# Kernel optimization log

Measured on AMD Instinct MI355X. Metric: run time of the kernel, lower is better.

The kernel has to match this reference:

```python
import jax, jax.numpy as jnp
import numpy as np

B, C, H, W = 2, 256, 360, 360
N1 = N2 = 1024


def setup_inputs() -> dict:
    key = jax.random.key(0)
    ks = jax.random.split(key, 12)
    s = 0.02
    feature = jax.random.normal(ks[0], (B, C, H, W), dtype=jnp.float32)
    # midx rows: [batch_idx, h, w]; frame 0 centers and frame 1 centers
    idx1 = jnp.stack([
        jnp.zeros((N1,), dtype=jnp.int32),
        jax.random.randint(ks[1], (N1,), 0, H, dtype=jnp.int32),
        jax.random.randint(ks[2], (N1,), 0, W, dtype=jnp.int32),
    ])
    idx2 = jnp.stack([
        jnp.ones((N2,), dtype=jnp.int32),
        jax.random.randint(ks[3], (N2,), 0, H, dtype=jnp.int32),
        jax.random.randint(ks[4], (N2,), 0, W, dtype=jnp.int32),
    ])
    w1 = jax.random.normal(ks[5], (256, 256), dtype=jnp.float32) * s
    b1 = jnp.zeros((256,), dtype=jnp.float32)
    w2 = jax.random.normal(ks[6], (256, 128), dtype=jnp.float32) * s
    b2 = jnp.zeros((128,), dtype=jnp.float32)
    w3 = jax.random.normal(ks[7], (128, 32), dtype=jnp.float32) * s
    b3 = jnp.zeros((32,), dtype=jnp.float32)
    w4 = jax.random.normal(ks[8], (32, 1), dtype=jnp.float32) * s
    b4 = jnp.zeros((1,), dtype=jnp.float32)
    return {"feature": feature, "idx1": idx1, "idx2": idx2,
            "w1": w1, "b1": b1, "w2": w2, "b2": b2,
            "w3": w3, "b3": b3, "w4": w4, "b4": b4}


def reference(feature, idx1, idx2, w1, b1, w2, b2, w3, b3, w4, b4):
    # feature: [B,C,H,W] -> [B,H,W,C] (torch .permute(0,2,3,1))
    feat = jnp.transpose(feature, (0, 2, 3, 1))

    def project(midx):
        # irregular gather of per-center features: [N, C]
        x = feat[midx[0], midx[1], midx[2]]
        h = jax.nn.relu(x @ w1 + b1)          # [N, 256]
        return jax.nn.relu(h @ w2 + b2)       # [N, 128]

    f1 = project(idx1)                        # [N1, D]
    f2 = project(idx2)                        # [N2, D]
    # laplacian_dists: broadcast outer difference [N1, N2, D]
    diff = f1[:, None, :] - f2[None, :, :]
    # out_layer = linear_last(D, 32, 1): Linear -> ReLU -> Linear
    h = jax.nn.relu(jnp.einsum('mnd,dk->mnk', diff, w3) + b3)
    out = jnp.einsum('mnk,ko->mno', h, w4) + b4
    return out[..., 0]                        # [N1, N2] similarity
```

## Files before the change

kernel.cpp:

```cpp
#include <hip/hip_runtime.h>

#define NPTS 1024
#define NC 256
#define NH 360
#define NW 360
#define NHW (NH * NW)
#define NCHW (NC * NHW)
#define PPB 4

__global__ __launch_bounds__(256) void mlp_kernel(
    const float* __restrict__ feature,
    const int* __restrict__ idx1,
    const int* __restrict__ idx2,
    const float* __restrict__ w1, const float* __restrict__ b1,
    const float* __restrict__ w2, const float* __restrict__ b2,
    const float* __restrict__ w3, const float* __restrict__ b3,
    float* __restrict__ pq)
{
    __shared__ float4 Xs[256];
    __shared__ float4 H1s[256];
    __shared__ float4 F2s[128];

    const int tid = threadIdx.x;
    const int base = blockIdx.x * PPB;

    {
        const int c = tid;
        const int col0 = base & (NPTS - 1);
        const int* idx = (base < NPTS) ? idx1 : idx2;
        const int4 bb4 = *(const int4*)(idx + col0);
        const int4 hh4 = *(const int4*)(idx + NPTS + col0);
        const int4 ww4 = *(const int4*)(idx + 2 * NPTS + col0);
        const size_t coff = (size_t)c * NHW;
        float4 v;
        v.x = __builtin_nontemporal_load(
                  feature + (size_t)bb4.x * NCHW + coff + (size_t)(hh4.x * NW + ww4.x));
        v.y = __builtin_nontemporal_load(
                  feature + (size_t)bb4.y * NCHW + coff + (size_t)(hh4.y * NW + ww4.y));
        v.z = __builtin_nontemporal_load(
                  feature + (size_t)bb4.z * NCHW + coff + (size_t)(hh4.z * NW + ww4.z));
        v.w = __builtin_nontemporal_load(
                  feature + (size_t)bb4.w * NCHW + coff + (size_t)(hh4.w * NW + ww4.w));
        Xs[c] = v;
    }
    __syncthreads();

    {
        const int j = tid;
        float4 acc = make_float4(0.f, 0.f, 0.f, 0.f);
        #pragma unroll 8
        for (int c = 0; c < 256; ++c) {
            const float wv = w1[c * 256 + j];
            const float4 a = Xs[c];
            acc.x = fmaf(a.x, wv, acc.x);
            acc.y = fmaf(a.y, wv, acc.y);
            acc.z = fmaf(a.z, wv, acc.z);
            acc.w = fmaf(a.w, wv, acc.w);
        }
        const float bj = b1[j];
        float4 h;
        h.x = fmaxf(acc.x + bj, 0.f);
        h.y = fmaxf(acc.y + bj, 0.f);
        h.z = fmaxf(acc.z + bj, 0.f);
        h.w = fmaxf(acc.w + bj, 0.f);
        H1s[j] = h;
    }
    __syncthreads();

    {
        const int j = tid & 127;
        const int ph = tid >> 7;
        const float* H1f = (const float*)H1s;
        float2 acc = make_float2(0.f, 0.f);
        #pragma unroll 8
        for (int c = 0; c < 256; ++c) {
            const float wv = w2[c * 128 + j];
            const float2 a = *(const float2*)&H1f[c * 4 + 2 * ph];
            acc.x = fmaf(a.x, wv, acc.x);
            acc.y = fmaf(a.y, wv, acc.y);
        }
        const float bj = b2[j];
        float* F2f = (float*)F2s;
        F2f[j * 4 + 2 * ph + 0] = fmaxf(acc.x + bj, 0.f);
        F2f[j * 4 + 2 * ph + 1] = fmaxf(acc.y + bj, 0.f);
    }
    __syncthreads();

    if (tid < 128) {
        const int j = tid & 31;
        const int g = tid >> 5;
        const float* F2f = (const float*)F2s;
        float acc = 0.f;
        #pragma unroll 8
        for (int c = 0; c < 128; ++c)
            acc = fmaf(F2f[c * 4 + g], w3[c * 32 + j], acc);
        const int point = base + g;
        const float val = (point < NPTS) ? acc : (b3[j] - acc);
        pq[(size_t)point * 32 + j] = val;
    }
}

#define MT 8

__global__ __launch_bounds__(256) void pair_kernel(
    const float* __restrict__ pq,
    const float* __restrict__ w4,
    const float* __restrict__ b4,
    float* __restrict__ out)
{
    const int tid = threadIdx.x;
    const int n = blockIdx.x * 256 + tid;
    const int m0 = blockIdx.y * MT;

    float q[32];
    const float4* q4 = (const float4*)(pq + (size_t)(NPTS + n) * 32);
    #pragma unroll
    for (int k8 = 0; k8 < 8; ++k8) {
        float4 t = q4[k8];
        q[4 * k8 + 0] = t.x;
        q[4 * k8 + 1] = t.y;
        q[4 * k8 + 2] = t.z;
        q[4 * k8 + 3] = t.w;
    }
    const float b4v = b4[0];

    #pragma unroll
    for (int mm = 0; mm < MT; ++mm) {
        const float* Pm = pq + (size_t)(m0 + mm) * 32;
        float a = b4v;
        #pragma unroll
        for (int k = 0; k < 32; ++k) {
            float t = Pm[k] + q[k];
            a = fmaf(w4[k], fmaxf(t, 0.f), a);
        }
        out[(size_t)(m0 + mm) * 1024 + n] = a;
    }
}

extern "C" void kernel_launch(void* const* d_in, const int* in_sizes, int n_in,
                              void* d_out, int out_size, void* d_ws, size_t ws_size,
                              hipStream_t stream) {
    const float* feature = (const float*)d_in[0];
    const int*   idx1    = (const int*)d_in[1];
    const int*   idx2    = (const int*)d_in[2];
    const float* w1      = (const float*)d_in[3];
    const float* b1      = (const float*)d_in[4];
    const float* w2      = (const float*)d_in[5];
    const float* b2      = (const float*)d_in[6];
    const float* w3      = (const float*)d_in[7];
    const float* b3      = (const float*)d_in[8];
    const float* w4      = (const float*)d_in[9];
    const float* b4      = (const float*)d_in[10];
    float* out = (float*)d_out;

    float* pq = (float*)d_ws;

    mlp_kernel<<<2048 / PPB, 256, 0, stream>>>(
        feature, idx1, idx2, w1, b1, w2, b2, w3, b3, pq);

    pair_kernel<<<dim3(4, 128), 256, 0, stream>>>(pq, w4, b4, out);
}
```

Before: 360.7 us.

## Run MLP projection with one wavefront per block and register-blocked outputs

The MLP kernel now launches 64 threads (one wavefront) per block instead of 256. Each lane gathers 16 feature values and computes 4 (layer 1) or 2 (layer 2) output columns, using float4/float2 weight loads. All __syncthreads calls are dropped, relying on a single wavefront executing LDS writes and reads in order. The aim is to cut barrier cost and issue wider, more reusable weight loads per FMA. The trade-off is 4x fewer waves to hide gather and L2 latency, and correctness now depends on implicit intra-wave LDS ordering.

```diff
diff --git a/kernel.cpp b/kernel.cpp
--- a/kernel.cpp
+++ b/kernel.cpp
@@ -8,7 +8,7 @@
 #define NCHW (NC * NHW)
 #define PPB 4
 
-__global__ __launch_bounds__(256) void mlp_kernel(
+__global__ __launch_bounds__(64) void mlp_kernel(
     const float* __restrict__ feature,
     const int* __restrict__ idx1,
     const int* __restrict__ idx2,
@@ -21,82 +21,107 @@
     __shared__ float4 H1s[256];
     __shared__ float4 F2s[128];
 
-    const int tid = threadIdx.x;
+    const int l = threadIdx.x;
     const int base = blockIdx.x * PPB;
 
     {
-        const int c = tid;
         const int col0 = base & (NPTS - 1);
         const int* idx = (base < NPTS) ? idx1 : idx2;
         const int4 bb4 = *(const int4*)(idx + col0);
         const int4 hh4 = *(const int4*)(idx + NPTS + col0);
         const int4 ww4 = *(const int4*)(idx + 2 * NPTS + col0);
-        const size_t coff = (size_t)c * NHW;
-        float4 v;
-        v.x = __builtin_nontemporal_load(
-                  feature + (size_t)bb4.x * NCHW + coff + (size_t)(hh4.x * NW + ww4.x));
-        v.y = __builtin_nontemporal_load(
-                  feature + (size_t)bb4.y * NCHW + coff + (size_t)(hh4.y * NW + ww4.y));
-        v.z = __builtin_nontemporal_load(
-                  feature + (size_t)bb4.z * NCHW + coff + (size_t)(hh4.z * NW + ww4.z));
-        v.w = __builtin_nontemporal_load(
-                  feature + (size_t)bb4.w * NCHW + coff + (size_t)(hh4.w * NW + ww4.w));
-        Xs[c] = v;
+        const size_t p0 = (size_t)bb4.x * NCHW + (size_t)(hh4.x * NW + ww4.x);
+        const size_t p1 = (size_t)bb4.y * NCHW + (size_t)(hh4.y * NW + ww4.y);
+        const size_t p2 = (size_t)bb4.z * NCHW + (size_t)(hh4.z * NW + ww4.z);
+        const size_t p3 = (size_t)bb4.w * NCHW + (size_t)(hh4.w * NW + ww4.w);
+        #pragma unroll
+        for (int k = 0; k < 4; ++k) {
+            const int c = l + 64 * k;
+            const size_t coff = (size_t)c * NHW;
+            float4 v;
+            v.x = __builtin_nontemporal_load(feature + p0 + coff);
+            v.y = __builtin_nontemporal_load(feature + p1 + coff);
+            v.z = __builtin_nontemporal_load(feature + p2 + coff);
+            v.w = __builtin_nontemporal_load(feature + p3 + coff);
+            Xs[c] = v;
+        }
     }
-    __syncthreads();
 
     {
-        const int j = tid;
-        float4 acc = make_float4(0.f, 0.f, 0.f, 0.f);
+        const float4* w1v = (const float4*)w1;
+        float4 a0 = {0,0,0,0}, a1 = {0,0,0,0}, a2 = {0,0,0,0}, a3 = {0,0,0,0};
         #pragma unroll 8
         for (int c = 0; c < 256; ++c) {
-            const float wv = w1[c * 256 + j];
-            const float4 a = Xs[c];
-            acc.x = fmaf(a.x, wv, acc.x);
-            acc.y = fmaf(a.y, wv, acc.y);
-            acc.z = fmaf(a.z, wv, acc.z);
-            acc.w = fmaf(a.w, wv, acc.w);
+            const float4 x = Xs[c];
+            const float4 w = w1v[c * 64 + l];
+            a0.x = fmaf(x.x, w.x, a0.x); a0.y = fmaf(x.y, w.x, a0.y);
+            a0.z = fmaf(x.z, w.x, a0.z); a0.w = fmaf(x.w, w.x, a0.w);
+            a1.x = fmaf(x.x, w.y, a1.x); a1.y = fmaf(x.y, w.y, a1.y);
+            a1.z = fmaf(x.z, w.y, a1.z); a1.w = fmaf(x.w, w.y, a1.w);
+            a2.x = fmaf(x.x, w.z, a2.x); a2.y = fmaf(x.y, w.z, a2.y);
+            a2.z = fmaf(x.z, w.z, a2.z); a2.w = fmaf(x.w, w.z, a2.w);
+            a3.x = fmaf(x.x, w.w, a3.x); a3.y = fmaf(x.y, w.w, a3.y);
+            a3.z = fmaf(x.z, w.w, a3.z); a3.w = fmaf(x.w, w.w, a3.w);
         }
-        const float bj = b1[j];
+        const float4 bb = ((const float4*)b1)[l];
         float4 h;
-        h.x = fmaxf(acc.x + bj, 0.f);
-        h.y = fmaxf(acc.y + bj, 0.f);
-        h.z = fmaxf(acc.z + bj, 0.f);
-        h.w = fmaxf(acc.w + bj, 0.f);
-        H1s[j] = h;
+        h.x = fmaxf(a0.x + bb.x, 0.f); h.y = fmaxf(a0.y + bb.x, 0.f);
+        h.z = fmaxf(a0.z + bb.x, 0.f); h.w = fmaxf(a0.w + bb.x, 0.f);
+        H1s[4 * l + 0] = h;
+        h.x = fmaxf(a1.x + bb.y, 0.f); h.y = fmaxf(a1.y + bb.y, 0.f);
+        h.z = fmaxf(a1.z + bb.y, 0.f); h.w = fmaxf(a1.w + bb.y, 0.f);
+        H1s[4 * l + 1] = h;
+        h.x = fmaxf(a2.x + bb.z, 0.f); h.y = fmaxf(a2.y + bb.z, 0.f);
+        h.z = fmaxf(a2.z + bb.z, 0.f); h.w = fmaxf(a2.w + bb.z, 0.f);
+        H1s[4 * l + 2] = h;
+        h.x = fmaxf(a3.x + bb.w, 0.f); h.y = fmaxf(a3.y + bb.w, 0.f);
+        h.z = fmaxf(a3.z + bb.w, 0.f); h.w = fmaxf(a3.w + bb.w, 0.f);
+        H1s[4 * l + 3] = h;
     }
-    __syncthreads();
 
     {
-        const int j = tid & 127;
-        const int ph = tid >> 7;
-        const float* H1f = (const float*)H1s;
-        float2 acc = make_float2(0.f, 0.f);
+        const float2* w2v = (const float2*)w2;
+        float4 a0 = {0,0,0,0}, a1 = {0,0,0,0};
         #pragma unroll 8
         for (int c = 0; c < 256; ++c) {
-            const float wv = w2[c * 128 + j];
-            const float2 a = *(const float2*)&H1f[c * 4 + 2 * ph];
-            acc.x = fmaf(a.x, wv, acc.x);
-            acc.y = fmaf(a.y, wv, acc.y);
+            const float4 x = H1s[c];
+            const float2 w = w2v[c * 64 + l];
+            a0.x = fmaf(x.x, w.x, a0.x); a0.y = fmaf(x.y, w.x, a0.y);
+            a0.z = fmaf(x.z, w.x, a0.z); a0.w = fmaf(x.w, w.x, a0.w);
+            a1.x = fmaf(x.x, w.y, a1.x); a1.y = fmaf(x.y, w.y, a1.y);
+            a1.z = fmaf(x.z, w.y, a1.z); a1.w = fmaf(x.w, w.y, a1.w);
         }
-        const float bj = b2[j];
-        float* F2f = (float*)F2s;
-        F2f[j * 4 + 2 * ph + 0] = fmaxf(acc.x + bj, 0.f);
-        F2f[j * 4 + 2 * ph + 1] = fmaxf(acc.y + bj, 0.f);
+        const float2 bb = ((const float2*)b2)[l];
+        float4 h;
+        h.x = fmaxf(a0.x + bb.x, 0.f); h.y = fmaxf(a0.y + bb.x, 0.f);
+        h.z = fmaxf(a0.z + bb.x, 0.f); h.w = fmaxf(a0.w + bb.x, 0.f);
+        F2s[2 * l + 0] = h;
+        h.x = fmaxf(a1.x + bb.y, 0.f); h.y = fmaxf(a1.y + bb.y, 0.f);
+        h.z = fmaxf(a1.z + bb.y, 0.f); h.w = fmaxf(a1.w + bb.y, 0.f);
+        F2s[2 * l + 1] = h;
     }
-    __syncthreads();
 
-    if (tid < 128) {
-        const int j = tid & 31;
-        const int g = tid >> 5;
+    {
+        const int j = l & 31;
+        const int gh = l >> 5;
         const float* F2f = (const float*)F2s;
-        float acc = 0.f;
+        float2 acc = {0.f, 0.f};
         #pragma unroll 8
-        for (int c = 0; c < 128; ++c)
-            acc = fmaf(F2f[c * 4 + g], w3[c * 32 + j], acc);
-        const int point = base + g;
-        const float val = (point < NPTS) ? acc : (b3[j] - acc);
-        pq[(size_t)point * 32 + j] = val;
+        for (int c = 0; c < 128; ++c) {
+            const float2 x = *(const float2*)&F2f[c * 4 + 2 * gh];
+            const float w = w3[c * 32 + j];
+            acc.x = fmaf(x.x, w, acc.x);
+            acc.y = fmaf(x.y, w, acc.y);
+        }
+        const int pA = base + 2 * gh;
+        if (base < NPTS) {
+            pq[(size_t)pA * 32 + j]       = acc.x;
+            pq[(size_t)(pA + 1) * 32 + j] = acc.y;
+        } else {
+            const float bj = b3[j];
+            pq[(size_t)pA * 32 + j]       = bj - acc.x;
+            pq[(size_t)(pA + 1) * 32 + j] = bj - acc.y;
+        }
     }
 }
 
@@ -155,7 +180,7 @@
 
     float* pq = (float*)d_ws;
 
-    mlp_kernel<<<2048 / PPB, 256, 0, stream>>>(
+    mlp_kernel<<<2048 / PPB, 64, 0, stream>>>(
         feature, idx1, idx2, w1, b1, w2, b2, w3, b3, pq);
 
     pair_kernel<<<dim3(4, 128), 256, 0, stream>>>(pq, w4, b4, out);
```

New measurement: 368.7 us. 2.2% more time.

## Split feature gather into separate kernel and pack pair loop into float2

Applied to the files above, without the earlier changes.

Moves the irregular feature gather out of the MLP kernel into its own kernel that writes the gathered vectors to workspace. The MLP kernel then reads them straight from global memory instead of staging them through shared memory behind a barrier. The pair kernel is rewritten with two-wide float vectors so the add, max and fma can map to packed FP32 instructions. This adds one kernel launch and a round trip through global memory for the gathered features.

```diff
diff --git a/kernel.cpp b/kernel.cpp
--- a/kernel.cpp
+++ b/kernel.cpp
@@ -6,70 +6,75 @@
 #define NW 360
 #define NHW (NH * NW)
 #define NCHW (NC * NHW)
-#define PPB 4
 
-__global__ __launch_bounds__(256) void mlp_kernel(
+typedef float v2f __attribute__((ext_vector_type(2)));
+
+__global__ __launch_bounds__(256) void gather_kernel(
     const float* __restrict__ feature,
     const int* __restrict__ idx1,
     const int* __restrict__ idx2,
+    float4* __restrict__ Xq)
+{
+    const int c = threadIdx.x;
+    const int quad = blockIdx.x;
+    const int base = quad * 4;
+    const int col0 = base & (NPTS - 1);
+    const int* idx = (base < NPTS) ? idx1 : idx2;
+    const int4 bb4 = *(const int4*)(idx + col0);
+    const int4 hh4 = *(const int4*)(idx + NPTS + col0);
+    const int4 ww4 = *(const int4*)(idx + 2 * NPTS + col0);
+    const size_t coff = (size_t)c * NHW;
+    float4 v;
+    v.x = __builtin_nontemporal_load(
+              feature + (size_t)bb4.x * NCHW + coff + (size_t)(hh4.x * NW + ww4.x));
+    v.y = __builtin_nontemporal_load(
+              feature + (size_t)bb4.y * NCHW + coff + (size_t)(hh4.y * NW + ww4.y));
+    v.z = __builtin_nontemporal_load(
+              feature + (size_t)bb4.z * NCHW + coff + (size_t)(hh4.z * NW + ww4.z));
+    v.w = __builtin_nontemporal_load(
+              feature + (size_t)bb4.w * NCHW + coff + (size_t)(hh4.w * NW + ww4.w));
+    Xq[(size_t)quad * 256 + c] = v;
+}
+
+__global__ __launch_bounds__(256) void mlp_kernel(
+    const float4* __restrict__ Xq,
     const float* __restrict__ w1, const float* __restrict__ b1,
     const float* __restrict__ w2, const float* __restrict__ b2,
     const float* __restrict__ w3, const float* __restrict__ b3,
     float* __restrict__ pq)
 {
-    __shared__ float4 Xs[256];
     __shared__ float4 H1s[256];
     __shared__ float4 F2s[128];
 
-    const int tid = threadIdx.x;
-    const int base = blockIdx.x * PPB;
+    const int t = threadIdx.x;
+    const int quad = blockIdx.x;
+    const int base = quad * 4;
+    const float4* __restrict__ Xr = Xq + (size_t)quad * 256;
 
     {
-        const int c = tid;
-        const int col0 = base & (NPTS - 1);
-        const int* idx = (base < NPTS) ? idx1 : idx2;
-        const int4 bb4 = *(const int4*)(idx + col0);
-        const int4 hh4 = *(const int4*)(idx + NPTS + col0);
-        const int4 ww4 = *(const int4*)(idx + 2 * NPTS + col0);
-        const size_t coff = (size_t)c * NHW;
-        float4 v;
-        v.x = __builtin_nontemporal_load(
-                  feature + (size_t)bb4.x * NCHW + coff + (size_t)(hh4.x * NW + ww4.x));
-        v.y = __builtin_nontemporal_load(
-                  feature + (size_t)bb4.y * NCHW + coff + (size_t)(hh4.y * NW + ww4.y));
-        v.z = __builtin_nontemporal_load(
-                  feature + (size_t)bb4.z * NCHW + coff + (size_t)(hh4.z * NW + ww4.z));
-        v.w = __builtin_nontemporal_load(
-                  feature + (size_t)bb4.w * NCHW + coff + (size_t)(hh4.w * NW + ww4.w));
-        Xs[c] = v;
-    }
-    __syncthreads();
-
-    {
-        const int j = tid;
         float4 acc = make_float4(0.f, 0.f, 0.f, 0.f);
         #pragma unroll 8
         for (int c = 0; c < 256; ++c) {
-            const float wv = w1[c * 256 + j];
-            const float4 a = Xs[c];
+            const float4 a = Xr[c];
+            const float wv = w1[c * 256 + t];
             acc.x = fmaf(a.x, wv, acc.x);
             acc.y = fmaf(a.y, wv, acc.y);
             acc.z = fmaf(a.z, wv, acc.z);
             acc.w = fmaf(a.w, wv, acc.w);
         }
-        const float bj = b1[j];
+        const float bj = b1[t];
         float4 h;
         h.x = fmaxf(acc.x + bj, 0.f);
         h.y = fmaxf(acc.y + bj, 0.f);
         h.z = fmaxf(acc.z + bj, 0.f);
         h.w = fmaxf(acc.w + bj, 0.f);
-        H1s[j] = h;
+        H1s[t] = h;
     }
     __syncthreads();
 
     {
-        const int j = tid & 127;
-        const int ph = tid >> 7;
+        const int j = t & 127;
+        const int ph = t >> 7;
         const float* H1f = (const float*)H1s;
         float2 acc = make_float2(0.f, 0.f);
         #pragma unroll 8
@@ -86,9 +91,9 @@
     }
     __syncthreads();
 
-    if (tid < 128) {
-        const int j = tid & 31;
-        const int g = tid >> 5;
+    if (t < 128) {
+        const int j = t & 31;
+        const int g = t >> 5;
         const float* F2f = (const float*)F2s;
         float acc = 0.f;
         #pragma unroll 8
@@ -112,28 +117,29 @@
     const int n = blockIdx.x * 256 + tid;
     const int m0 = blockIdx.y * MT;
 
-    float q[32];
+    v2f q[16];
     const float4* q4 = (const float4*)(pq + (size_t)(NPTS + n) * 32);
     #pragma unroll
     for (int k8 = 0; k8 < 8; ++k8) {
-        float4 t = q4[k8];
-        q[4 * k8 + 0] = t.x;
-        q[4 * k8 + 1] = t.y;
-        q[4 * k8 + 2] = t.z;
-        q[4 * k8 + 3] = t.w;
+        float4 v = q4[k8];
+        q[2 * k8 + 0] = (v2f){v.x, v.y};
+        q[2 * k8 + 1] = (v2f){v.z, v.w};
     }
     const float b4v = b4[0];
+    const v2f zero = {0.f, 0.f};
 
     #pragma unroll
     for (int mm = 0; mm < MT; ++mm) {
-        const float* Pm = pq + (size_t)(m0 + mm) * 32;
-        float a = b4v;
+        const v2f* Pm = (const v2f*)(pq + (size_t)(m0 + mm) * 32);
+        const v2f* w4v = (const v2f*)w4;
+        v2f acc = {b4v, 0.f};
         #pragma unroll
-        for (int k = 0; k < 32; ++k) {
-            float t = Pm[k] + q[k];
-            a = fmaf(w4[k], fmaxf(t, 0.f), a);
+        for (int k2 = 0; k2 < 16; ++k2) {
+            v2f tv = Pm[k2] + q[k2];
+            v2f rv = __builtin_elementwise_max(tv, zero);
+            acc = __builtin_elementwise_fma(w4v[k2], rv, acc);
         }
-        out[(size_t)(m0 + mm) * 1024 + n] = a;
+        out[(size_t)(m0 + mm) * 1024 + n] = acc.x + acc.y;
     }
 }
 
@@ -153,10 +159,10 @@
     const float* b4      = (const float*)d_in[10];
     float* out = (float*)d_out;
 
-    float* pq = (float*)d_ws;
+    float*  pq = (float*)d_ws;
+    float4* Xq = (float4*)((char*)d_ws + 256 * 1024);
 
-    mlp_kernel<<<2048 / PPB, 256, 0, stream>>>(
-        feature, idx1, idx2, w1, b1, w2, b2, w3, b3, pq);
-
+    gather_kernel<<<512, 256, 0, stream>>>(feature, idx1, idx2, Xq);
+    mlp_kernel<<<512, 256, 0, stream>>>(Xq, w1, b1, w2, b2, w3, b3, pq);
     pair_kernel<<<dim3(4, 128), 256, 0, stream>>>(pq, w4, b4, out);
 }
```

Measured after the change: 363.1 us. Within noise of the previous version (+0.6%).
